# Kernel optimization log

Hardware: AMD Instinct MI355X
Metric: run time of the kernel (lower is better)

## Reference

```python
import jax, jax.numpy as jnp
import numpy as np

T1 = 8      # list[index-1]
T2 = 8      # list[index]
L = 8
GAMA = 1.0
EPS = -8e-05

@jax.custom_vjp
def zif(u):
    return (u >= EPS).astype(u.dtype)

def _zif_fwd(u):
    return zif(u), u

def _zif_bwd(u, g):
    tmp = (1.0 / GAMA) * (1.0 / GAMA) * jnp.clip(GAMA - jnp.abs(u), a_min=0.0)
    return (g * tmp,)

zif.defvjp(_zif_fwd, _zif_bwd)


def setup_inputs() -> dict:
    key = jax.random.key(0)
    k1, k2 = jax.random.split(key)
    x = jax.random.uniform(k1, (T1 * 32, 128, 32, 32), dtype=jnp.float32)
    thresh = jnp.ones((1,), dtype=jnp.float32)  # nn.Parameter([1.0])
    return {"x": x, "thresh": thresh}


def _if_forward(x, thresh):
    # thre = thresh.data / L  (detached in the original)
    thre = jax.lax.stop_gradient(thresh) / L          # [1]
    # expand: [T1*B, C, H, W] -> [T1, B, C, H, W]
    B = x.shape[0] // T1
    x_seq = x.reshape((T1, B) + x.shape[1:])
    frame_shape = x_seq.shape[1:]

    mem0 = jnp.broadcast_to(0.5 * thre, frame_shape).astype(x.dtype)
    sc0 = jnp.zeros(frame_shape, dtype=x.dtype)

    # Phase 1: integrate-and-fire over the T1 input frames
    def step1(carry, xt):
        mem, sc = carry
        mem = mem + xt
        spike = zif(mem - thre) * thre
        mem = mem - spike
        return (mem, sc + spike), None
    (mem, sc), _ = jax.lax.scan(step1, (mem0, sc0), x_seq)

    # Phase 2: T3-1 relaxation steps with reverse spikes (hard, no surrogate)
    T3 = max(T1, T2)
    def step2(carry, _):
        mem, sc = carry
        spike = zif(mem - thre) * thre
        rev = (-mem > 0).astype(mem.dtype) * thre
        mem = mem - spike + rev
        return (mem, sc + spike - rev), None
    (mem, sc), _ = jax.lax.scan(step2, (mem, sc), None, length=T3 - 1)

    # Phase 3: re-emit spike_count as T2 output spikes
    def step3(mem, _):
        spike = zif(mem - thre) * thre
        return mem - spike, spike
    _, spike_pot = jax.lax.scan(step3, sc, None, length=T2)  # [T2, B, C, H, W]

    # merge: flatten(0, 1)
    return spike_pot.reshape((T2 * B,) + frame_shape[1:])


def reference(x, thresh):
    return _if_forward(x, thresh)
```

## Files before the change

### kernel.cpp

```cpp
#include <hip/hip_runtime.h>


#define T1 8
#define T2 8
#define L_DIV 8.0f
#define EPS_C (-8e-05f)

typedef float fvec4 __attribute__((ext_vector_type(4)));

__global__ __launch_bounds__(256) void if_phase12_kernel(
    const fvec4* __restrict__ x,
    const float* __restrict__ thresh,
    fvec4* __restrict__ sc_out,
    int n4)
{
    const int i = blockIdx.x * blockDim.x + threadIdx.x;
    const float thre = thresh[0] / L_DIV;

    const fvec4* a0 = &x[(size_t)0 * n4 + i];
    const fvec4* a1 = &x[(size_t)1 * n4 + i];
    const fvec4* a2 = &x[(size_t)2 * n4 + i];
    const fvec4* a3 = &x[(size_t)3 * n4 + i];
    const fvec4* a4 = &x[(size_t)4 * n4 + i];
    const fvec4* a5 = &x[(size_t)5 * n4 + i];
    const fvec4* a6 = &x[(size_t)6 * n4 + i];
    const fvec4* a7 = &x[(size_t)7 * n4 + i];

    fvec4 xv[T1];
    asm volatile(
        "global_load_dwordx4 %0, %8, off\n\t"
        "global_load_dwordx4 %1, %9, off\n\t"
        "global_load_dwordx4 %2, %10, off\n\t"
        "global_load_dwordx4 %3, %11, off\n\t"
        "global_load_dwordx4 %4, %12, off\n\t"
        "global_load_dwordx4 %5, %13, off\n\t"
        "global_load_dwordx4 %6, %14, off\n\t"
        "global_load_dwordx4 %7, %15, off\n\t"
        "s_waitcnt vmcnt(0)"
        : "=&v"(xv[0]), "=&v"(xv[1]), "=&v"(xv[2]), "=&v"(xv[3]),
          "=&v"(xv[4]), "=&v"(xv[5]), "=&v"(xv[6]), "=&v"(xv[7])
        : "v"(a0), "v"(a1), "v"(a2), "v"(a3),
          "v"(a4), "v"(a5), "v"(a6), "v"(a7)
        : "memory");

    float m[4], sc[4];
    #pragma unroll
    for (int k = 0; k < 4; ++k) { m[k] = 0.5f * thre; sc[k] = 0.0f; }

    #pragma unroll
    for (int t = 0; t < T1; ++t) {
        #pragma unroll
        for (int k = 0; k < 4; ++k) {
            m[k] += xv[t][k];
            const float spike = (m[k] - thre >= EPS_C) ? thre : 0.0f;
            m[k] -= spike;
            sc[k] += spike;
        }
    }

    #pragma unroll
    for (int t = 0; t < T1 - 1; ++t) {
        #pragma unroll
        for (int k = 0; k < 4; ++k) {
            const float spike = (m[k] - thre >= EPS_C) ? thre : 0.0f;
            const float rev   = (-m[k] > 0.0f) ? thre : 0.0f;
            m[k] = m[k] - spike + rev;
            sc[k] += spike - rev;
        }
    }

    fvec4 o;
    #pragma unroll
    for (int k = 0; k < 4; ++k) o[k] = sc[k];
    sc_out[i] = o;
}

__global__ __launch_bounds__(256) void if_phase3_kernel(
    const fvec4* __restrict__ sc_in,
    const float* __restrict__ thresh,
    fvec4* __restrict__ out,
    int n4)
{
    const int bid = blockIdx.x;
    const int t   = bid >> 10;
    const int s   = bid & 1023;
    const int base = s * 1024 + threadIdx.x;

    const float thre = thresh[0] / L_DIV;
    const float cut  = (float)(t + 1) * thre;

    fvec4* outt = out + (size_t)t * n4;

    #pragma unroll
    for (int c = 0; c < 4; ++c) {
        const int i = base + c * 256;
        const fvec4 scv = sc_in[i];
        fvec4 o;
        #pragma unroll
        for (int k = 0; k < 4; ++k) {
            o[k] = (scv[k] - cut >= EPS_C) ? thre : 0.0f;
        }
        __builtin_nontemporal_store(o, &outt[i]);
    }
}

#define G 2
__global__ __launch_bounds__(256) void if_fused_kernel(
    const fvec4* __restrict__ x,
    const float* __restrict__ thresh,
    fvec4* __restrict__ out,
    int n4)
{
    const int base = blockIdx.x * (blockDim.x * G) + threadIdx.x;
    const float thre = thresh[0] / L_DIV;

    fvec4 xv[G][T1];
    #pragma unroll
    for (int t = 0; t < T1; ++t)
        #pragma unroll
        for (int g = 0; g < G; ++g)
            xv[g][t] = x[(size_t)t * n4 + base + g * 256];

    float m[G][4], sc[G][4];
    #pragma unroll
    for (int g = 0; g < G; ++g)
        #pragma unroll
        for (int k = 0; k < 4; ++k) { m[g][k] = 0.5f * thre; sc[g][k] = 0.0f; }

    #pragma unroll
    for (int t = 0; t < T1; ++t)
        #pragma unroll
        for (int g = 0; g < G; ++g)
            #pragma unroll
            for (int k = 0; k < 4; ++k) {
                m[g][k] += xv[g][t][k];
                const float spike = (m[g][k] - thre >= EPS_C) ? thre : 0.0f;
                m[g][k] -= spike;
                sc[g][k] += spike;
            }

    #pragma unroll
    for (int t = 0; t < T1 - 1; ++t)
        #pragma unroll
        for (int g = 0; g < G; ++g)
            #pragma unroll
            for (int k = 0; k < 4; ++k) {
                const float spike = (m[g][k] - thre >= EPS_C) ? thre : 0.0f;
                const float rev   = (-m[g][k] > 0.0f) ? thre : 0.0f;
                m[g][k] = m[g][k] - spike + rev;
                sc[g][k] += spike - rev;
            }

    #pragma unroll
    for (int t = 0; t < T2; ++t)
        #pragma unroll
        for (int g = 0; g < G; ++g) {
            fvec4 o;
            #pragma unroll
            for (int k = 0; k < 4; ++k) {
                const float spike = (sc[g][k] - thre >= EPS_C) ? thre : 0.0f;
                o[k] = spike;
                sc[g][k] -= spike;
            }
            __builtin_nontemporal_store(o, &out[(size_t)t * n4 + base + g * 256]);
        }
}

extern "C" void kernel_launch(void* const* d_in, const int* in_sizes, int n_in,
                              void* d_out, int out_size, void* d_ws, size_t ws_size,
                              hipStream_t stream) {
    const fvec4* x      = (const fvec4*)d_in[0];
    const float* thresh = (const float*)d_in[1];
    fvec4*       out    = (fvec4*)d_out;

    const int N  = in_sizes[0] / T1;
    const int n4 = N / 4;
    const int block = 256;

    const size_t sc_bytes = (size_t)N * sizeof(float);

    if (ws_size >= sc_bytes) {
        fvec4* sc = (fvec4*)d_ws;
        if_phase12_kernel<<<n4 / block, block, 0, stream>>>(x, thresh, sc, n4);
        if_phase3_kernel<<<(n4 / 1024) * T2, block, 0, stream>>>(sc, thresh, out, n4);
    } else {
        if_fused_kernel<<<n4 / (block * G), block, 0, stream>>>(x, thresh, out, n4);
    }
}
```

Baseline: 243.5 us.

## Software-pipeline time-step loads in phase-1/2 kernel with two vectors per thread

```diff
diff --git a/kernel.cpp b/kernel.cpp
--- a/kernel.cpp
+++ b/kernel.cpp
@@ -8,71 +8,66 @@
 
 typedef float fvec4 __attribute__((ext_vector_type(4)));
 
-__global__ __launch_bounds__(256) void if_phase12_kernel(
+__global__ __launch_bounds__(256) void if_phase12_sweep(
     const fvec4* __restrict__ x,
     const float* __restrict__ thresh,
     fvec4* __restrict__ sc_out,
     int n4)
 {
-    const int i = blockIdx.x * blockDim.x + threadIdx.x;
+    const int base = blockIdx.x * 512 + threadIdx.x;
     const float thre = thresh[0] / L_DIV;
 
-    const fvec4* a0 = &x[(size_t)0 * n4 + i];
-    const fvec4* a1 = &x[(size_t)1 * n4 + i];
-    const fvec4* a2 = &x[(size_t)2 * n4 + i];
-    const fvec4* a3 = &x[(size_t)3 * n4 + i];
-    const fvec4* a4 = &x[(size_t)4 * n4 + i];
-    const fvec4* a5 = &x[(size_t)5 * n4 + i];
-    const fvec4* a6 = &x[(size_t)6 * n4 + i];
-    const fvec4* a7 = &x[(size_t)7 * n4 + i];
+    float m[2][4], sc[2][4];
+    #pragma unroll
+    for (int g = 0; g < 2; ++g)
+        #pragma unroll
+        for (int k = 0; k < 4; ++k) { m[g][k] = 0.5f * thre; sc[g][k] = 0.0f; }
 
-    fvec4 xv[T1];
-    asm volatile(
-        "global_load_dwordx4 %0, %8, off\n\t"
-        "global_load_dwordx4 %1, %9, off\n\t"
-        "global_load_dwordx4 %2, %10, off\n\t"
-        "global_load_dwordx4 %3, %11, off\n\t"
-        "global_load_dwordx4 %4, %12, off\n\t"
-        "global_load_dwordx4 %5, %13, off\n\t"
-        "global_load_dwordx4 %6, %14, off\n\t"
-        "global_load_dwordx4 %7, %15, off\n\t"
-        "s_waitcnt vmcnt(0)"
-        : "=&v"(xv[0]), "=&v"(xv[1]), "=&v"(xv[2]), "=&v"(xv[3]),
-          "=&v"(xv[4]), "=&v"(xv[5]), "=&v"(xv[6]), "=&v"(xv[7])
-        : "v"(a0), "v"(a1), "v"(a2), "v"(a3),
-          "v"(a4), "v"(a5), "v"(a6), "v"(a7)
-        : "memory");
-
-    float m[4], sc[4];
-    #pragma unroll
-    for (int k = 0; k < 4; ++k) { m[k] = 0.5f * thre; sc[k] = 0.0f; }
+    fvec4 cur0 = x[base];
+    fvec4 cur1 = x[base + 256];
 
     #pragma unroll
     for (int t = 0; t < T1; ++t) {
+        fvec4 nxt0, nxt1;
+        if (t < T1 - 1) {
+            nxt0 = x[(size_t)(t + 1) * n4 + base];
+            nxt1 = x[(size_t)(t + 1) * n4 + base + 256];
+        }
         #pragma unroll
         for (int k = 0; k < 4; ++k) {
-            m[k] += xv[t][k];
-            const float spike = (m[k] - thre >= EPS_C) ? thre : 0.0f;
-            m[k] -= spike;
-            sc[k] += spike;
+            m[0][k] += cur0[k];
+            float spike = (m[0][k] - thre >= EPS_C) ? thre : 0.0f;
+            m[0][k] -= spike;
+            sc[0][k] += spike;
+
+            m[1][k] += cur1[k];
+            spike = (m[1][k] - thre >= EPS_C) ? thre : 0.0f;
+            m[1][k] -= spike;
+            sc[1][k] += spike;
         }
+        __syncthreads();
+        cur0 = nxt0;
+        cur1 = nxt1;
     }
 
     #pragma unroll
     for (int t = 0; t < T1 - 1; ++t) {
         #pragma unroll
-        for (int k = 0; k < 4; ++k) {
-            const float spike = (m[k] - thre >= EPS_C) ? thre : 0.0f;
-            const float rev   = (-m[k] > 0.0f) ? thre : 0.0f;
-            m[k] = m[k] - spike + rev;
-            sc[k] += spike - rev;
-        }
+        for (int g = 0; g < 2; ++g)
+            #pragma unroll
+            for (int k = 0; k < 4; ++k) {
+                const float spike = (m[g][k] - thre >= EPS_C) ? thre : 0.0f;
+                const float rev   = (-m[g][k] > 0.0f) ? thre : 0.0f;
+                m[g][k] = m[g][k] - spike + rev;
+                sc[g][k] += spike - rev;
+            }
     }
 
-    fvec4 o;
+    fvec4 o0, o1;
     #pragma unroll
-    for (int k = 0; k < 4; ++k) o[k] = sc[k];
-    sc_out[i] = o;
+    for (int k = 0; k < 4; ++k) { o0[k] = sc[0][k]; o1[k] = sc[1][k]; }
+    sc_out[base]       = o0;
+    sc_out[base + 256] = o1;
 }
 
 __global__ __launch_bounds__(256) void if_phase3_kernel(
@@ -181,7 +176,7 @@
 
     if (ws_size >= sc_bytes) {
         fvec4* sc = (fvec4*)d_ws;
-        if_phase12_kernel<<<n4 / block, block, 0, stream>>>(x, thresh, sc, n4);
+        if_phase12_sweep<<<n4 / 512, block, 0, stream>>>(x, thresh, sc, n4);
         if_phase3_kernel<<<(n4 / 1024) * T2, block, 0, stream>>>(sc, thresh, out, n4);
     } else {
         if_fused_kernel<<<n4 / (block * G), block, 0, stream>>>(x, thresh, out, n4);
```

Measured after the change: 237.8 us. 1.02x faster.
